# Kernel optimization log

Hardware: AMD Instinct MI355X
Metric: run time of the kernel (lower is better)

## Reference

```python
import jax, jax.numpy as jnp
import numpy as np

NQ = 8          # num_qubits
NL = 3          # num_layers
B = 65536       # batch size (vectorized over the original per-sample loop)
DIM = 2 ** NQ   # 256 state-vector amplitudes

# Pauli-Z eigenvalues per qubit over the computational basis (wire 0 = MSB,
# matching pennylane default.qubit ordering): ZV[q, idx] in {+1, -1}.
_idx = np.arange(DIM)
ZV = np.stack([1.0 - 2.0 * ((_idx >> (NQ - 1 - q)) & 1) for q in range(NQ)]).astype(np.float32)  # (NQ, DIM)
ZZ = ZV[:-1] * ZV[1:]   # (NQ-1, DIM): Z_i Z_{i+1} diagonal for the CNOT-RZ-CNOT (=RZZ) blocks


def setup_inputs() -> dict:
    key = jax.random.key(0)
    k1, k2, k3 = jax.random.split(key, 3)
    # weights ~ U(-pi, pi), matching torch.rand(...)*2*pi - pi
    weights = jax.random.uniform(k1, (NL, 2 * NQ - 1), minval=-np.pi, maxval=np.pi, dtype=jnp.float32)
    # latent noise ~ U(-1, 1), matching torch.rand(batch)*2 - 1
    z1 = jax.random.uniform(k2, (B,), minval=-1.0, maxval=1.0, dtype=jnp.float32)
    z2 = jax.random.uniform(k3, (B,), minval=-1.0, maxval=1.0, dtype=jnp.float32)
    return {"weights": weights, "z1": z1, "z2": z2}


def _apply_ry(state, theta, q):
    """Apply RY(theta) on wire q of state shaped (B, 2, ..., 2)."""
    half = theta * 0.5
    co, si = jnp.cos(half), jnp.sin(half)
    U = jnp.stack([jnp.stack([co, -si]), jnp.stack([si, co])]).astype(state.dtype)  # (2,2)
    s = jnp.moveaxis(state, q + 1, -1)
    s = s @ U.T
    return jnp.moveaxis(s, -1, q + 1)


def _circuit(weights, z1, z2):
    # Initial layer: per qubit RY(arcsin(z1)) then RZ(arcsin(z2)) on |0>
    # -> single-qubit state [e^{-i a2/2} cos(a1/2), e^{+i a2/2} sin(a1/2)], identical on all wires.
    a1 = jnp.arcsin(z1)
    a2 = jnp.arcsin(z2)
    ph = jnp.exp(-0.5j * a2)                              # (B,) complex64
    v = jnp.stack([ph * jnp.cos(0.5 * a1),
                   jnp.conj(ph) * jnp.sin(0.5 * a1)], axis=-1).astype(jnp.complex64)  # (B, 2)
    # Product state across NQ wires: (B, 2^NQ)
    state = v
    for _ in range(NQ - 1):
        state = (state[:, :, None] * v[:, None, :]).reshape(state.shape[0], -1)
    state = state.reshape((-1,) + (2,) * NQ)

    zz = jnp.asarray(ZZ)
    for l in range(NL):
        for q in range(NQ):
            state = _apply_ry(state, weights[l, q], q)
        # Entangling block: CNOT(i,i+1) RZ(w) CNOT(i,i+1) == RZZ(w) on (i,i+1),
        # all diagonal -> fuse the whole block into one phase multiply.
        angle = weights[l, NQ:] @ zz                      # (DIM,)
        diag = jnp.exp(-0.5j * angle).reshape((2,) * NQ)
        state = state * diag

    probs = jnp.abs(state.reshape(state.shape[0], -1)) ** 2   # (B, DIM)
    return (probs @ jnp.asarray(ZV).T).astype(jnp.float32)    # (B, NQ) <Z_q> expectations


def reference(weights, z1, z2):
    return _circuit(weights, z1, z2)
```

## Files before the change

kernel.cpp:

```cpp
#include <hip/hip_runtime.h>


#define ROW 92

template <int CTRL>
__device__ __forceinline__ float dppf(float x) {
    return __int_as_float(
        __builtin_amdgcn_mov_dpp(__float_as_int(x), CTRL, 0xF, 0xF, true));
}
template <int PAT>
__device__ __forceinline__ float swzp(float x) {
    return __int_as_float(__builtin_amdgcn_ds_swizzle(__float_as_int(x), PAT));
}
template <int B>
__device__ __forceinline__ float lane_xor(float x) {
    if constexpr (B == 0) return dppf<0xB1>(x);
    else if constexpr (B == 1) return dppf<0x4E>(x);
    else if constexpr (B == 2) return swzp<0x101F>(x);
    else if constexpr (B == 3) return dppf<0x128>(x);
    else if constexpr (B == 4) return swzp<0x401F>(x);
    else return __shfl_xor(x, 32, 64);
}

__device__ __forceinline__ void gate_lds2_5(float2 Cv[5], float2 (*xch)[256],
                                            float2 cs0, float2 cs1,
                                            int j, int M0) {
    __syncthreads();
    #pragma unroll
    for (int m = 0; m < 5; ++m) xch[M0 + m][j] = Cv[m];
    __syncthreads();
    const float s0 = (j & 128) ? cs0.y : -cs0.y;
    const float s1 = (j & 64)  ? cs1.y : -cs1.y;
    const float a00 = cs0.x * cs1.x, a01 = cs0.x * s1;
    const float a10 = s0 * cs1.x,    a11 = s0 * s1;
    #pragma unroll
    for (int m = 0; m < 5; ++m) {
        const float2 p01 = xch[M0 + m][j ^ 64];
        const float2 p10 = xch[M0 + m][j ^ 128];
        const float2 p11 = xch[M0 + m][j ^ 192];
        Cv[m].x = a00 * Cv[m].x + a01 * p01.x + a10 * p10.x + a11 * p11.x;
        Cv[m].y = a00 * Cv[m].y + a01 * p01.y + a10 * p10.y + a11 * p11.y;
    }
}

template <int B>
__device__ __forceinline__ void gate_wave5(float2 Cv[5], float2 cs, int j) {
    const float sg = ((j >> B) & 1) ? cs.y : -cs.y;
    #pragma unroll
    for (int m = 0; m < 5; ++m) {
        const float pr = lane_xor<B>(Cv[m].x);
        const float pi = lane_xor<B>(Cv[m].y);
        Cv[m].x = cs.x * Cv[m].x + sg * pr;
        Cv[m].y = cs.x * Cv[m].y + sg * pi;
    }
}

template <int N>
__device__ __forceinline__ void wht_chunk(float (&v)[N], float* buf,
                                          int lane, int wvg, int row, int base) {
    #define WHT_LVL(B)                                                   \
    {                                                                    \
        const float sgn = ((lane >> (B)) & 1) ? -1.f : 1.f;              \
        _Pragma("unroll")                                                \
        for (int i = 0; i < N; ++i) {                                    \
            const float p = lane_xor<B>(v[i]);                           \
            v[i] = fmaf(sgn, v[i], p);                                   \
        }                                                                \
    }
    WHT_LVL(0) WHT_LVL(1) WHT_LVL(2) WHT_LVL(3) WHT_LVL(4) WHT_LVL(5)
    #undef WHT_LVL
    if (row >= 0) {
        #pragma unroll
        for (int i = 0; i < N; ++i) buf[(wvg * 7 + row) * 81 + base + i] = v[i];
    }
}

template <int D, int N>
__device__ __forceinline__ void fill_pairs(const float2 (&C9)[9], float (&c)[N],
                                           int off) {
    #pragma unroll
    for (int k = 0; k + D <= 8; ++k) {
        const float2 hi = C9[k + D], lo = C9[k];
        c[off + 2 * k]     = 2.f * (hi.x * lo.x + hi.y * lo.y);
        c[off + 2 * k + 1] = 2.f * (hi.y * lo.x - hi.x * lo.y);
    }
}

__device__ __forceinline__ void prep(float z1v, float z2v, float& u, float& w8,
                                     float Tr[9], float Ti[9]) {
    const float u1 = sqrtf(fmaxf(0.f, 1.f - z1v * z1v));
    const float q1 = 0.5f * (1.f + u1);
    const float s1 = copysignf(sqrtf(fmaxf(0.f, 0.5f * (1.f - u1))), z1v);
    const float tn = s1 * rsqrtf(q1);
    const float u2 = sqrtf(fmaxf(0.f, 1.f - z2v * z2v));
    const float tr = tn * u2, ti = tn * z2v;
    u = tn * tn;
    w8 = q1 * q1; w8 *= w8; w8 *= w8;
    Tr[1] = tr; Ti[1] = ti;
    #pragma unroll
    for (int d = 2; d <= 8; ++d) {
        Tr[d] = Tr[d - 1] * tr - Ti[d - 1] * ti;
        Ti[d] = Tr[d - 1] * ti + Ti[d - 1] * tr;
    }
}

__device__ __forceinline__ float apoly1(const float* gp, float u) {
    const float4 c0 = ((const float4*)gp)[0];
    const float4 c1 = ((const float4*)gp)[1];
    const float4 c2 = ((const float4*)gp)[2];
    const float a[9] = {c0.x, c0.y, c0.z, c0.w, c1.x, c1.y, c1.z, c1.w, c2.x};
    float r = a[8];
    #pragma unroll
    for (int m = 7; m >= 0; --m) r = fmaf(r, u, a[m]);
    return r;
}

template <int NP>
__device__ __forceinline__ float2 bpoly1(const float* gp, float u) {
    constexpr int NF4 = (2 * NP + 3) / 4;
    float4 c[NF4];
    const float4* p = (const float4*)gp;
    #pragma unroll
    for (int i = 0; i < NF4; ++i) c[i] = p[i];
    float br = 0.f, bi = 0.f;
    #pragma unroll
    for (int k = NP - 1; k >= 0; --k) {
        const float re = (k & 1) ? c[k >> 1].z : c[k >> 1].x;
        const float im = (k & 1) ? c[k >> 1].w : c[k >> 1].y;
        br = fmaf(br, u, re);
        bi = fmaf(bi, u, im);
    }
    return make_float2(br, bi);
}

__global__ __launch_bounds__(512, 2)
void qsim_fused(const float* __restrict__ w, const float* __restrict__ z1,
                const float* __restrict__ z2, float* __restrict__ out,
                int nsamp) {
    __shared__ float2 xch[9][256];
    __shared__ float2 s_cs[3][8];
    __shared__ __align__(16) float g[8 * ROW];

    const int t = threadIdx.x;
    const int j = t & 255;
    const int h = t >> 8;
    const int M0 = h * 4;
    const int lane = t & 63, wvg = (t >> 6) & 3;

    const int s = blockIdx.x * 256 + j;
    const bool ev = (s < nsamp);
    float u = 0.f, w8 = 0.f;
    float Tr[9], Ti[9];
    if (ev) prep(z1[s], z2[s], u, w8, Tr, Ti);

    if (t < 24) {
        int l = t >> 3, q = t & 7;
        float a = 0.5f * w[l * 15 + q];
        s_cs[l][q] = make_float2(__cosf(a), __sinf(a));
    }
    __syncthreads();

    float2 Cv[5];
    #pragma unroll
    for (int m = 0; m < 5; ++m)
        Cv[m] = make_float2((__popc(j) == M0 + m) ? 1.f : 0.f, 0.f);

    for (int l = 0; l < 3; ++l) {
        gate_lds2_5(Cv, xch, s_cs[l][0], s_cs[l][1], j, M0);
        gate_wave5<5>(Cv, s_cs[l][2], j);
        gate_wave5<4>(Cv, s_cs[l][3], j);
        gate_wave5<3>(Cv, s_cs[l][4], j);
        gate_wave5<2>(Cv, s_cs[l][5], j);
        gate_wave5<1>(Cv, s_cs[l][6], j);
        gate_wave5<0>(Cv, s_cs[l][7], j);
        if (l < 2) {
            float ang = 0.f;
            #pragma unroll
            for (int i = 0; i < 7; ++i) {
                float zz = (((j >> (7 - i)) ^ (j >> (6 - i))) & 1) ? -1.f : 1.f;
                ang = fmaf(w[l * 15 + 8 + i], zz, ang);
            }
            float s2, c2;
            __sincosf(0.5f * ang, &s2, &c2);
            #pragma unroll
            for (int m = 0; m < 5; ++m) {
                const float nr = Cv[m].x * c2 + Cv[m].y * s2;
                const float ni = Cv[m].y * c2 - Cv[m].x * s2;
                Cv[m].x = nr; Cv[m].y = ni;
            }
        }
    }

    __syncthreads();
    #pragma unroll
    for (int m = 0; m < 5; ++m) xch[M0 + m][j] = Cv[m];
    __syncthreads();
    float2 C9[9];
    #pragma unroll
    for (int m = 0; m < 9; ++m) C9[m] = xch[m][j];
    __syncthreads();

    float* buf = (float*)xch + h * (28 * 81);
    const int row = (lane == 0) ? 0 : (lane == 1) ? 1 : (lane == 2) ? 2 :
                    (lane == 4) ? 3 : (lane == 8) ? 4 : (lane == 16) ? 5 :
                    (lane == 32) ? 6 : -1;
    if (h == 0) {
        {   float c[9];
            #pragma unroll
            for (int m = 0; m < 9; ++m)
                c[m] = C9[m].x * C9[m].x + C9[m].y * C9[m].y;
            wht_chunk(c, buf, lane, wvg, row, 0);
        }
        { float c[16]; fill_pairs<1>(C9, c, 0); wht_chunk(c, buf, lane, wvg, row, 9);  }
        { float c[14]; fill_pairs<2>(C9, c, 0); wht_chunk(c, buf, lane, wvg, row, 25); }
    } else {
        { float c[12]; fill_pairs<3>(C9, c, 0); wht_chunk(c, buf, lane, wvg, row, 39); }
        { float c[10]; fill_pairs<4>(C9, c, 0); wht_chunk(c, buf, lane, wvg, row, 51); }
        { float c[8];  fill_pairs<5>(C9, c, 0); wht_chunk(c, buf, lane, wvg, row, 61); }
        {   float c[12];
            fill_pairs<6>(C9, c, 0);
            fill_pairs<7>(C9, c, 6);
            fill_pairs<8>(C9, c, 10);
            wht_chunk(c, buf, lane, wvg, row, 69);
        }
    }
    __syncthreads();
    for (int o = t; o < 648; o += 512) {
        const int q = o / 81, i = o - 81 * q;
        const int b = 7 - q;
        const float* gb = (const float*)xch + ((i < 39) ? 0 : 28 * 81);
        float r;
        if (b < 6) {
            const int rw = b + 1;
            r = gb[(0 * 7 + rw) * 81 + i] + gb[(1 * 7 + rw) * 81 + i] +
                gb[(2 * 7 + rw) * 81 + i] + gb[(3 * 7 + rw) * 81 + i];
        } else if (b == 6) {
            r = gb[(0 * 7) * 81 + i] - gb[(1 * 7) * 81 + i] +
                gb[(2 * 7) * 81 + i] - gb[(3 * 7) * 81 + i];
        } else {
            r = gb[(0 * 7) * 81 + i] + gb[(1 * 7) * 81 + i] -
                gb[(2 * 7) * 81 + i] - gb[(3 * 7) * 81 + i];
        }
        const int off = i + ((i < 9) ? 0 : (i < 39) ? 3 : (i < 61) ? 5 :
                             (i < 75) ? 7 : 9);
        g[q * ROW + off] = r;
    }
    __syncthreads();

    if (!ev) return;

    float o4[4];
    #pragma unroll
    for (int qq = 0; qq < 4; ++qq) {
        const float* gq = g + (M0 + qq) * ROW;
        float r = apoly1(gq, u);
        #define DTERM(D, NP, OFF)                                        \
        {                                                                \
            const float2 b = bpoly1<NP>(gq + OFF, u);                    \
            r = fmaf(Tr[D], b.x, r);                                     \
            r = fmaf(-Ti[D], b.y, r);                                    \
        }
        DTERM(1, 8, 12) DTERM(2, 7, 28) DTERM(3, 6, 44) DTERM(4, 5, 56)
        DTERM(5, 4, 68) DTERM(6, 3, 76) DTERM(7, 2, 84) DTERM(8, 1, 88)
        #undef DTERM
        o4[qq] = w8 * r;
    }

    float4* op = (float4*)(out + (size_t)s * 8 + M0);
    *op = make_float4(o4[0], o4[1], o4[2], o4[3]);
}

extern "C" void kernel_launch(void* const* d_in, const int* in_sizes, int n_in,
                              void* d_out, int out_size, void* d_ws,
                              size_t ws_size, hipStream_t stream) {
    const float* w  = (const float*)d_in[0];
    const float* z1 = (const float*)d_in[1];
    const float* z2 = (const float*)d_in[2];
    float* out = (float*)d_out;

    const int n = in_sizes[1];
    qsim_fused<<<(n + 255) / 256, 512, 0, stream>>>(w, z1, z2, out, n);
}
```

Measured before the change: 16.30 us.

## Split work across four 256-thread groups with 1024-thread blocks

Raises the block size from 512 to 1024 threads so each group of 256 threads carries fewer Hamming-weight slices (3 instead of 5) during the gate simulation. The Walsh-Hadamard chunks are redistributed over four groups, and each thread evaluates two output qubits instead of four. The per-sample prep is moved after the reduction so fewer registers stay live. This adds per-thread parallelism and cuts register pressure, but it duplicates some work (the slice arrays overlap between groups), makes launch bounds much tighter, and uses larger blocks with more barrier participants.

```diff
diff --git a/kernel.cpp b/kernel.cpp
--- a/kernel.cpp
+++ b/kernel.cpp
@@ -22,19 +22,19 @@
     else return __shfl_xor(x, 32, 64);
 }
 
-__device__ __forceinline__ void gate_lds2_5(float2 Cv[5], float2 (*xch)[256],
+__device__ __forceinline__ void gate_lds2_3(float2 Cv[3], float2 (*xch)[256],
                                             float2 cs0, float2 cs1,
                                             int j, int M0) {
     __syncthreads();
     #pragma unroll
-    for (int m = 0; m < 5; ++m) xch[M0 + m][j] = Cv[m];
+    for (int m = 0; m < 3; ++m) xch[M0 + m][j] = Cv[m];
     __syncthreads();
     const float s0 = (j & 128) ? cs0.y : -cs0.y;
     const float s1 = (j & 64)  ? cs1.y : -cs1.y;
     const float a00 = cs0.x * cs1.x, a01 = cs0.x * s1;
     const float a10 = s0 * cs1.x,    a11 = s0 * s1;
     #pragma unroll
-    for (int m = 0; m < 5; ++m) {
+    for (int m = 0; m < 3; ++m) {
         const float2 p01 = xch[M0 + m][j ^ 64];
         const float2 p10 = xch[M0 + m][j ^ 128];
         const float2 p11 = xch[M0 + m][j ^ 192];
@@ -44,10 +44,10 @@
 }
 
 template <int B>
-__device__ __forceinline__ void gate_wave5(float2 Cv[5], float2 cs, int j) {
+__device__ __forceinline__ void gate_wave3(float2 Cv[3], float2 cs, int j) {
     const float sg = ((j >> B) & 1) ? cs.y : -cs.y;
     #pragma unroll
-    for (int m = 0; m < 5; ++m) {
+    for (int m = 0; m < 3; ++m) {
         const float pr = lane_xor<B>(Cv[m].x);
         const float pi = lane_xor<B>(Cv[m].y);
         Cv[m].x = cs.x * Cv[m].x + sg * pr;
@@ -133,7 +133,7 @@
     return make_float2(br, bi);
 }
 
-__global__ __launch_bounds__(512, 2)
+__global__ __launch_bounds__(1024, 4)
 void qsim_fused(const float* __restrict__ w, const float* __restrict__ z1,
                 const float* __restrict__ z2, float* __restrict__ out,
                 int nsamp) {
@@ -144,14 +144,13 @@
     const int t = threadIdx.x;
     const int j = t & 255;
     const int h = t >> 8;
-    const int M0 = h * 4;
+    const int M0 = 2 * h;
     const int lane = t & 63, wvg = (t >> 6) & 3;
 
     const int s = blockIdx.x * 256 + j;
     const bool ev = (s < nsamp);
-    float u = 0.f, w8 = 0.f;
-    float Tr[9], Ti[9];
-    if (ev) prep(z1[s], z2[s], u, w8, Tr, Ti);
+    const float z1v = ev ? z1[s] : 0.f;
+    const float z2v = ev ? z2[s] : 0.f;
 
     if (t < 24) {
         int l = t >> 3, q = t & 7;
@@ -160,19 +159,19 @@
     }
     __syncthreads();
 
-    float2 Cv[5];
-    #pragma unroll
-    for (int m = 0; m < 5; ++m)
+    float2 Cv[3];
+    #pragma unroll
+    for (int m = 0; m < 3; ++m)
         Cv[m] = make_float2((__popc(j) == M0 + m) ? 1.f : 0.f, 0.f);
 
     for (int l = 0; l < 3; ++l) {
-        gate_lds2_5(Cv, xch, s_cs[l][0], s_cs[l][1], j, M0);
-        gate_wave5<5>(Cv, s_cs[l][2], j);
-        gate_wave5<4>(Cv, s_cs[l][3], j);
-        gate_wave5<3>(Cv, s_cs[l][4], j);
-        gate_wave5<2>(Cv, s_cs[l][5], j);
-        gate_wave5<1>(Cv, s_cs[l][6], j);
-        gate_wave5<0>(Cv, s_cs[l][7], j);
+        gate_lds2_3(Cv, xch, s_cs[l][0], s_cs[l][1], j, M0);
+        gate_wave3<5>(Cv, s_cs[l][2], j);
+        gate_wave3<4>(Cv, s_cs[l][3], j);
+        gate_wave3<3>(Cv, s_cs[l][4], j);
+        gate_wave3<2>(Cv, s_cs[l][5], j);
+        gate_wave3<1>(Cv, s_cs[l][6], j);
+        gate_wave3<0>(Cv, s_cs[l][7], j);
         if (l < 2) {
             float ang = 0.f;
             #pragma unroll
@@ -183,7 +182,7 @@
             float s2, c2;
             __sincosf(0.5f * ang, &s2, &c2);
             #pragma unroll
-            for (int m = 0; m < 5; ++m) {
+            for (int m = 0; m < 3; ++m) {
                 const float nr = Cv[m].x * c2 + Cv[m].y * s2;
                 const float ni = Cv[m].y * c2 - Cv[m].x * s2;
                 Cv[m].x = nr; Cv[m].y = ni;
@@ -193,14 +192,14 @@
 
     __syncthreads();
     #pragma unroll
-    for (int m = 0; m < 5; ++m) xch[M0 + m][j] = Cv[m];
+    for (int m = 0; m < 3; ++m) xch[M0 + m][j] = Cv[m];
     __syncthreads();
     float2 C9[9];
     #pragma unroll
     for (int m = 0; m < 9; ++m) C9[m] = xch[m][j];
     __syncthreads();
 
-    float* buf = (float*)xch + h * (28 * 81);
+    float* buf = (float*)xch;
     const int row = (lane == 0) ? 0 : (lane == 1) ? 1 : (lane == 2) ? 2 :
                     (lane == 4) ? 3 : (lane == 8) ? 4 : (lane == 16) ? 5 :
                     (lane == 32) ? 6 : -1;
@@ -211,35 +210,34 @@
                 c[m] = C9[m].x * C9[m].x + C9[m].y * C9[m].y;
             wht_chunk(c, buf, lane, wvg, row, 0);
         }
+        { float c[12]; fill_pairs<3>(C9, c, 0); wht_chunk(c, buf, lane, wvg, row, 39); }
+    } else if (h == 1) {
         { float c[16]; fill_pairs<1>(C9, c, 0); wht_chunk(c, buf, lane, wvg, row, 9);  }
+        { float c[2];  fill_pairs<8>(C9, c, 0); wht_chunk(c, buf, lane, wvg, row, 79); }
+    } else if (h == 2) {
         { float c[14]; fill_pairs<2>(C9, c, 0); wht_chunk(c, buf, lane, wvg, row, 25); }
+        { float c[6];  fill_pairs<6>(C9, c, 0); wht_chunk(c, buf, lane, wvg, row, 69); }
     } else {
-        { float c[12]; fill_pairs<3>(C9, c, 0); wht_chunk(c, buf, lane, wvg, row, 39); }
         { float c[10]; fill_pairs<4>(C9, c, 0); wht_chunk(c, buf, lane, wvg, row, 51); }
         { float c[8];  fill_pairs<5>(C9, c, 0); wht_chunk(c, buf, lane, wvg, row, 61); }
-        {   float c[12];
-            fill_pairs<6>(C9, c, 0);
-            fill_pairs<7>(C9, c, 6);
-            fill_pairs<8>(C9, c, 10);
-            wht_chunk(c, buf, lane, wvg, row, 69);
-        }
-    }
-    __syncthreads();
-    for (int o = t; o < 648; o += 512) {
+        { float c[4];  fill_pairs<7>(C9, c, 0); wht_chunk(c, buf, lane, wvg, row, 75); }
+    }
+    __syncthreads();
+    if (t < 648) {
+        const int o = t;
         const int q = o / 81, i = o - 81 * q;
         const int b = 7 - q;
-        const float* gb = (const float*)xch + ((i < 39) ? 0 : 28 * 81);
         float r;
         if (b < 6) {
             const int rw = b + 1;
-            r = gb[(0 * 7 + rw) * 81 + i] + gb[(1 * 7 + rw) * 81 + i] +
-                gb[(2 * 7 + rw) * 81 + i] + gb[(3 * 7 + rw) * 81 + i];
+            r = buf[(0 * 7 + rw) * 81 + i] + buf[(1 * 7 + rw) * 81 + i] +
+                buf[(2 * 7 + rw) * 81 + i] + buf[(3 * 7 + rw) * 81 + i];
         } else if (b == 6) {
-            r = gb[(0 * 7) * 81 + i] - gb[(1 * 7) * 81 + i] +
-                gb[(2 * 7) * 81 + i] - gb[(3 * 7) * 81 + i];
+            r = buf[(0 * 7) * 81 + i] - buf[(1 * 7) * 81 + i] +
+                buf[(2 * 7) * 81 + i] - buf[(3 * 7) * 81 + i];
         } else {
-            r = gb[(0 * 7) * 81 + i] + gb[(1 * 7) * 81 + i] -
-                gb[(2 * 7) * 81 + i] - gb[(3 * 7) * 81 + i];
+            r = buf[(0 * 7) * 81 + i] + buf[(1 * 7) * 81 + i] -
+                buf[(2 * 7) * 81 + i] - buf[(3 * 7) * 81 + i];
         }
         const int off = i + ((i < 9) ? 0 : (i < 39) ? 3 : (i < 61) ? 5 :
                              (i < 75) ? 7 : 9);
@@ -249,10 +247,14 @@
 
     if (!ev) return;
 
-    float o4[4];
-    #pragma unroll
-    for (int qq = 0; qq < 4; ++qq) {
-        const float* gq = g + (M0 + qq) * ROW;
+    float u, w8;
+    float Tr[9], Ti[9];
+    prep(z1v, z2v, u, w8, Tr, Ti);
+
+    float o2[2];
+    #pragma unroll
+    for (int k = 0; k < 2; ++k) {
+        const float* gq = g + (M0 + k) * ROW;
         float r = apoly1(gq, u);
         #define DTERM(D, NP, OFF)                                        \
         {                                                                \
@@ -263,11 +265,11 @@
         DTERM(1, 8, 12) DTERM(2, 7, 28) DTERM(3, 6, 44) DTERM(4, 5, 56)
         DTERM(5, 4, 68) DTERM(6, 3, 76) DTERM(7, 2, 84) DTERM(8, 1, 88)
         #undef DTERM
-        o4[qq] = w8 * r;
-    }
-
-    float4* op = (float4*)(out + (size_t)s * 8 + M0);
-    *op = make_float4(o4[0], o4[1], o4[2], o4[3]);
+        o2[k] = w8 * r;
+    }
+
+    float2* op = (float2*)(out + (size_t)s * 8 + M0);
+    *op = make_float2(o2[0], o2[1]);
 }
 
 extern "C" void kernel_launch(void* const* d_in, const int* in_sizes, int n_in,
@@ -279,5 +281,5 @@
     float* out = (float*)d_out;
 
     const int n = in_sizes[1];
-    qsim_fused<<<(n + 255) / 256, 512, 0, stream>>>(w, z1, z2, out, n);
-}
+    qsim_fused<<<(n + 255) / 256, 1024, 0, stream>>>(w, z1, z2, out, n);
+}
```

Measured after the change: 16.77 us. 2.9% more time.

## Remap final polynomial stage to one qubit per thread over four samples

Applied to the files above, without the earlier changes.

The final evaluation stage is remapped so each thread handles one qubit for four consecutive samples, instead of four qubits for one sample. The thread loads that qubit's coefficient row from shared memory into registers once and reuses it for all four samples. z1/z2 are now read as float4 vectors and the per-sample prep is recomputed four times per thread. The cost is about four times more redundant prep work, a 92-float register array under a 512x2 launch bound (risk of spills), and narrower scattered output stores. A partially filled last group of four samples would see zero inputs rather than the real ones.

```diff
diff --git a/kernel.cpp b/kernel.cpp
--- a/kernel.cpp
+++ b/kernel.cpp
@@ -104,35 +104,6 @@
     }
 }
 
-__device__ __forceinline__ float apoly1(const float* gp, float u) {
-    const float4 c0 = ((const float4*)gp)[0];
-    const float4 c1 = ((const float4*)gp)[1];
-    const float4 c2 = ((const float4*)gp)[2];
-    const float a[9] = {c0.x, c0.y, c0.z, c0.w, c1.x, c1.y, c1.z, c1.w, c2.x};
-    float r = a[8];
-    #pragma unroll
-    for (int m = 7; m >= 0; --m) r = fmaf(r, u, a[m]);
-    return r;
-}
-
-template <int NP>
-__device__ __forceinline__ float2 bpoly1(const float* gp, float u) {
-    constexpr int NF4 = (2 * NP + 3) / 4;
-    float4 c[NF4];
-    const float4* p = (const float4*)gp;
-    #pragma unroll
-    for (int i = 0; i < NF4; ++i) c[i] = p[i];
-    float br = 0.f, bi = 0.f;
-    #pragma unroll
-    for (int k = NP - 1; k >= 0; --k) {
-        const float re = (k & 1) ? c[k >> 1].z : c[k >> 1].x;
-        const float im = (k & 1) ? c[k >> 1].w : c[k >> 1].y;
-        br = fmaf(br, u, re);
-        bi = fmaf(bi, u, im);
-    }
-    return make_float2(br, bi);
-}
-
 __global__ __launch_bounds__(512, 2)
 void qsim_fused(const float* __restrict__ w, const float* __restrict__ z1,
                 const float* __restrict__ z2, float* __restrict__ out,
@@ -147,11 +118,15 @@
     const int M0 = h * 4;
     const int lane = t & 63, wvg = (t >> 6) & 3;
 
-    const int s = blockIdx.x * 256 + j;
-    const bool ev = (s < nsamp);
-    float u = 0.f, w8 = 0.f;
-    float Tr[9], Ti[9];
-    if (ev) prep(z1[s], z2[s], u, w8, Tr, Ti);
+    const int gidx = t >> 3;
+    const int sbase = blockIdx.x * 256 + gidx * 4;
+    const bool ev4 = (sbase + 3 < nsamp);
+    float4 z1v4 = make_float4(0.f, 0.f, 0.f, 0.f);
+    float4 z2v4 = z1v4;
+    if (ev4) {
+        z1v4 = *(const float4*)(z1 + sbase);
+        z2v4 = *(const float4*)(z2 + sbase);
+    }
 
     if (t < 24) {
         int l = t >> 3, q = t & 7;
@@ -247,27 +222,58 @@
     }
     __syncthreads();
 
-    if (!ev) return;
-
+    const int q = t & 7;
+    const float* gq = g + q * ROW;
+
+    float a[ROW];
+    #pragma unroll
+    for (int i = 0; i < 23; ++i) {
+        const float4 c = ((const float4*)gq)[i];
+        a[4 * i + 0] = c.x; a[4 * i + 1] = c.y;
+        a[4 * i + 2] = c.z; a[4 * i + 3] = c.w;
+    }
+
+    const float z1a[4] = {z1v4.x, z1v4.y, z1v4.z, z1v4.w};
+    const float z2a[4] = {z2v4.x, z2v4.y, z2v4.z, z2v4.w};
     float o4[4];
-    #pragma unroll
-    for (int qq = 0; qq < 4; ++qq) {
-        const float* gq = g + (M0 + qq) * ROW;
-        float r = apoly1(gq, u);
+
+    #pragma unroll
+    for (int i = 0; i < 4; ++i) {
+        float u, w8;
+        float Tr[9], Ti[9];
+        prep(z1a[i], z2a[i], u, w8, Tr, Ti);
+
+        float r = a[8];
+        #pragma unroll
+        for (int m = 7; m >= 0; --m) r = fmaf(r, u, a[m]);
+
         #define DTERM(D, NP, OFF)                                        \
         {                                                                \
-            const float2 b = bpoly1<NP>(gq + OFF, u);                    \
-            r = fmaf(Tr[D], b.x, r);                                     \
-            r = fmaf(-Ti[D], b.y, r);                                    \
+            float br = a[OFF + 2 * (NP - 1)];                            \
+            float bi = a[OFF + 2 * (NP - 1) + 1];                        \
+            _Pragma("unroll")                                            \
+            for (int k = NP - 2; k >= 0; --k) {                          \
+                br = fmaf(br, u, a[OFF + 2 * k]);                        \
+                bi = fmaf(bi, u, a[OFF + 2 * k + 1]);                    \
+            }                                                            \
+            r = fmaf(Tr[D], br, r);                                      \
+            r = fmaf(-Ti[D], bi, r);                                     \
         }
         DTERM(1, 8, 12) DTERM(2, 7, 28) DTERM(3, 6, 44) DTERM(4, 5, 56)
         DTERM(5, 4, 68) DTERM(6, 3, 76) DTERM(7, 2, 84) DTERM(8, 1, 88)
         #undef DTERM
-        o4[qq] = w8 * r;
-    }
-
-    float4* op = (float4*)(out + (size_t)s * 8 + M0);
-    *op = make_float4(o4[0], o4[1], o4[2], o4[3]);
+        o4[i] = w8 * r;
+    }
+
+    if (ev4) {
+        #pragma unroll
+        for (int i = 0; i < 4; ++i)
+            out[(size_t)(sbase + i) * 8 + q] = o4[i];
+    } else {
+        #pragma unroll
+        for (int i = 0; i < 4; ++i)
+            if (sbase + i < nsamp) out[(size_t)(sbase + i) * 8 + q] = o4[i];
+    }
 }
 
 extern "C" void kernel_launch(void* const* d_in, const int* in_sizes, int n_in,
```

Measured after the change: 16.27 us. Within noise of the previous version (-0.2%).

## Distribute weight-polynomial state evolution over nine waves with in-register qubit pairs

Applied to the files above, without the earlier changes.

Restructures the circuit-evolution stage so each of nine waves (576 threads) owns one Hamming-weight column and holds four amplitudes per lane. The top two qubits are applied in registers via pair rotations instead of an LDS exchange with two barriers per layer. The ZZ phase is built from precomputed cos/sin products rather than an angle sum plus sincos. Per-sample prep is also deferred until after the shared reduction, which lowers register pressure during evolution. This removes per-layer syncthreads and redundant five-slot work per thread, at the cost of a larger block, a separate WHT buffer in LDS, and an idle 9th wave in later phases.

```diff
diff --git a/kernel.cpp b/kernel.cpp
--- a/kernel.cpp
+++ b/kernel.cpp
@@ -22,37 +22,27 @@
     else return __shfl_xor(x, 32, 64);
 }
 
-__device__ __forceinline__ void gate_lds2_5(float2 Cv[5], float2 (*xch)[256],
-                                            float2 cs0, float2 cs1,
-                                            int j, int M0) {
-    __syncthreads();
-    #pragma unroll
-    for (int m = 0; m < 5; ++m) xch[M0 + m][j] = Cv[m];
-    __syncthreads();
-    const float s0 = (j & 128) ? cs0.y : -cs0.y;
-    const float s1 = (j & 64)  ? cs1.y : -cs1.y;
-    const float a00 = cs0.x * cs1.x, a01 = cs0.x * s1;
-    const float a10 = s0 * cs1.x,    a11 = s0 * s1;
-    #pragma unroll
-    for (int m = 0; m < 5; ++m) {
-        const float2 p01 = xch[M0 + m][j ^ 64];
-        const float2 p10 = xch[M0 + m][j ^ 128];
-        const float2 p11 = xch[M0 + m][j ^ 192];
-        Cv[m].x = a00 * Cv[m].x + a01 * p01.x + a10 * p10.x + a11 * p11.x;
-        Cv[m].y = a00 * Cv[m].y + a01 * p01.y + a10 * p10.y + a11 * p11.y;
-    }
+__device__ __forceinline__ float2 cmul(float2 a, float2 b) {
+    return make_float2(a.x * b.x - a.y * b.y, a.x * b.y + a.y * b.x);
 }
 
 template <int B>
-__device__ __forceinline__ void gate_wave5(float2 Cv[5], float2 cs, int j) {
-    const float sg = ((j >> B) & 1) ? cs.y : -cs.y;
-    #pragma unroll
-    for (int m = 0; m < 5; ++m) {
-        const float pr = lane_xor<B>(Cv[m].x);
-        const float pi = lane_xor<B>(Cv[m].y);
-        Cv[m].x = cs.x * Cv[m].x + sg * pr;
-        Cv[m].y = cs.x * Cv[m].y + sg * pi;
-    }
+__device__ __forceinline__ void gate_lane(float2 CA[4], float2 cs, int lane) {
+    const float sg = ((lane >> B) & 1) ? cs.y : -cs.y;
+    #pragma unroll
+    for (int r = 0; r < 4; ++r) {
+        const float px = lane_xor<B>(CA[r].x);
+        const float py = lane_xor<B>(CA[r].y);
+        CA[r].x = cs.x * CA[r].x + sg * px;
+        CA[r].y = cs.x * CA[r].y + sg * py;
+    }
+}
+__device__ __forceinline__ void gate_pair(float2& a0, float2& a1, float2 cs) {
+    const float2 t0 = make_float2(cs.x * a0.x - cs.y * a1.x,
+                                  cs.x * a0.y - cs.y * a1.y);
+    const float2 t1 = make_float2(cs.y * a0.x + cs.x * a1.x,
+                                  cs.y * a0.y + cs.x * a1.y);
+    a0 = t0; a1 = t1;
 }
 
 template <int N>
@@ -133,102 +123,114 @@
     return make_float2(br, bi);
 }
 
-__global__ __launch_bounds__(512, 2)
+__global__ __launch_bounds__(576, 3)
 void qsim_fused(const float* __restrict__ w, const float* __restrict__ z1,
                 const float* __restrict__ z2, float* __restrict__ out,
                 int nsamp) {
-    __shared__ float2 xch[9][256];
-    __shared__ float2 s_cs[3][8];
+    __shared__ float2 xchC[9][256];
+    __shared__ float wht[2 * 28 * 81];
+    __shared__ float2 s_cs[3][15];
     __shared__ __align__(16) float g[8 * ROW];
 
     const int t = threadIdx.x;
+    const int lane = t & 63;
+    const int wv = t >> 6;
     const int j = t & 255;
-    const int h = t >> 8;
+    const int h = (t >> 8) & 1;
     const int M0 = h * 4;
-    const int lane = t & 63, wvg = (t >> 6) & 3;
 
     const int s = blockIdx.x * 256 + j;
-    const bool ev = (s < nsamp);
-    float u = 0.f, w8 = 0.f;
-    float Tr[9], Ti[9];
-    if (ev) prep(z1[s], z2[s], u, w8, Tr, Ti);
-
-    if (t < 24) {
-        int l = t >> 3, q = t & 7;
-        float a = 0.5f * w[l * 15 + q];
-        s_cs[l][q] = make_float2(__cosf(a), __sinf(a));
-    }
-    __syncthreads();
-
-    float2 Cv[5];
-    #pragma unroll
-    for (int m = 0; m < 5; ++m)
-        Cv[m] = make_float2((__popc(j) == M0 + m) ? 1.f : 0.f, 0.f);
-
+    const bool ev = (t < 512) && (s < nsamp);
+    const float z1v = ev ? z1[s] : 0.f;
+    const float z2v = ev ? z2[s] : 0.f;
+
+    if (t < 45) {
+        const int l = t / 15, i = t - 15 * l;
+        const float a = 0.5f * w[l * 15 + i];
+        s_cs[l][i] = make_float2(__cosf(a), __sinf(a));
+    }
+    __syncthreads();
+
+    float2 CA[4];
+    const int pl = __popc(lane);
+    #pragma unroll
+    for (int r = 0; r < 4; ++r)
+        CA[r] = make_float2((pl + (r >> 1) + (r & 1) == wv) ? 1.f : 0.f, 0.f);
+
+    #pragma unroll 1
     for (int l = 0; l < 3; ++l) {
-        gate_lds2_5(Cv, xch, s_cs[l][0], s_cs[l][1], j, M0);
-        gate_wave5<5>(Cv, s_cs[l][2], j);
-        gate_wave5<4>(Cv, s_cs[l][3], j);
-        gate_wave5<3>(Cv, s_cs[l][4], j);
-        gate_wave5<2>(Cv, s_cs[l][5], j);
-        gate_wave5<1>(Cv, s_cs[l][6], j);
-        gate_wave5<0>(Cv, s_cs[l][7], j);
+        gate_pair(CA[0], CA[2], s_cs[l][0]);
+        gate_pair(CA[1], CA[3], s_cs[l][0]);
+        gate_pair(CA[0], CA[1], s_cs[l][1]);
+        gate_pair(CA[2], CA[3], s_cs[l][1]);
+        gate_lane<5>(CA, s_cs[l][2], lane);
+        gate_lane<4>(CA, s_cs[l][3], lane);
+        gate_lane<3>(CA, s_cs[l][4], lane);
+        gate_lane<2>(CA, s_cs[l][5], lane);
+        gate_lane<1>(CA, s_cs[l][6], lane);
+        gate_lane<0>(CA, s_cs[l][7], lane);
         if (l < 2) {
-            float ang = 0.f;
+            float2 base = make_float2(1.f, 0.f);
             #pragma unroll
-            for (int i = 0; i < 7; ++i) {
-                float zz = (((j >> (7 - i)) ^ (j >> (6 - i))) & 1) ? -1.f : 1.f;
-                ang = fmaf(w[l * 15 + 8 + i], zz, ang);
-            }
-            float s2, c2;
-            __sincosf(0.5f * ang, &s2, &c2);
+            for (int i = 2; i <= 6; ++i) {
+                const float2 cz = s_cs[l][8 + i];
+                const int d = ((lane >> (7 - i)) ^ (lane >> (6 - i))) & 1;
+                base = cmul(base, make_float2(cz.x, d ? cz.y : -cz.y));
+            }
+            const float2 cz0 = s_cs[l][8];
+            const float2 cz1 = s_cs[l][9];
+            const int l5 = (lane >> 5) & 1;
             #pragma unroll
-            for (int m = 0; m < 5; ++m) {
-                const float nr = Cv[m].x * c2 + Cv[m].y * s2;
-                const float ni = Cv[m].y * c2 - Cv[m].x * s2;
-                Cv[m].x = nr; Cv[m].y = ni;
-            }
-        }
-    }
-
-    __syncthreads();
-    #pragma unroll
-    for (int m = 0; m < 5; ++m) xch[M0 + m][j] = Cv[m];
-    __syncthreads();
-    float2 C9[9];
-    #pragma unroll
-    for (int m = 0; m < 9; ++m) C9[m] = xch[m][j];
-    __syncthreads();
-
-    float* buf = (float*)xch + h * (28 * 81);
-    const int row = (lane == 0) ? 0 : (lane == 1) ? 1 : (lane == 2) ? 2 :
-                    (lane == 4) ? 3 : (lane == 8) ? 4 : (lane == 16) ? 5 :
-                    (lane == 32) ? 6 : -1;
-    if (h == 0) {
-        {   float c[9];
-            #pragma unroll
-            for (int m = 0; m < 9; ++m)
-                c[m] = C9[m].x * C9[m].x + C9[m].y * C9[m].y;
-            wht_chunk(c, buf, lane, wvg, row, 0);
-        }
-        { float c[16]; fill_pairs<1>(C9, c, 0); wht_chunk(c, buf, lane, wvg, row, 9);  }
-        { float c[14]; fill_pairs<2>(C9, c, 0); wht_chunk(c, buf, lane, wvg, row, 25); }
-    } else {
-        { float c[12]; fill_pairs<3>(C9, c, 0); wht_chunk(c, buf, lane, wvg, row, 39); }
-        { float c[10]; fill_pairs<4>(C9, c, 0); wht_chunk(c, buf, lane, wvg, row, 51); }
-        { float c[8];  fill_pairs<5>(C9, c, 0); wht_chunk(c, buf, lane, wvg, row, 61); }
-        {   float c[12];
-            fill_pairs<6>(C9, c, 0);
-            fill_pairs<7>(C9, c, 6);
-            fill_pairs<8>(C9, c, 10);
-            wht_chunk(c, buf, lane, wvg, row, 69);
-        }
-    }
-    __syncthreads();
-    for (int o = t; o < 648; o += 512) {
+            for (int r = 0; r < 4; ++r) {
+                const int d0 = ((r >> 1) ^ (r & 1)) & 1;
+                const int d1 = (r & 1) ^ l5;
+                float2 ph = cmul(base, make_float2(cz0.x, d0 ? cz0.y : -cz0.y));
+                ph = cmul(ph, make_float2(cz1.x, d1 ? cz1.y : -cz1.y));
+                CA[r] = cmul(CA[r], ph);
+            }
+        }
+    }
+
+    #pragma unroll
+    for (int r = 0; r < 4; ++r) xchC[wv][r * 64 + lane] = CA[r];
+    __syncthreads();
+
+    const int wvg = (t >> 6) & 3;
+    if (t < 512) {
+        float2 C9[9];
+        #pragma unroll
+        for (int m = 0; m < 9; ++m) C9[m] = xchC[m][j];
+        float* buf = wht + h * (28 * 81);
+        const int row = (lane == 0) ? 0 : (lane == 1) ? 1 : (lane == 2) ? 2 :
+                        (lane == 4) ? 3 : (lane == 8) ? 4 : (lane == 16) ? 5 :
+                        (lane == 32) ? 6 : -1;
+        if (h == 0) {
+            {   float c[9];
+                #pragma unroll
+                for (int m = 0; m < 9; ++m)
+                    c[m] = C9[m].x * C9[m].x + C9[m].y * C9[m].y;
+                wht_chunk(c, buf, lane, wvg, row, 0);
+            }
+            { float c[16]; fill_pairs<1>(C9, c, 0); wht_chunk(c, buf, lane, wvg, row, 9);  }
+            { float c[14]; fill_pairs<2>(C9, c, 0); wht_chunk(c, buf, lane, wvg, row, 25); }
+        } else {
+            { float c[12]; fill_pairs<3>(C9, c, 0); wht_chunk(c, buf, lane, wvg, row, 39); }
+            { float c[10]; fill_pairs<4>(C9, c, 0); wht_chunk(c, buf, lane, wvg, row, 51); }
+            { float c[8];  fill_pairs<5>(C9, c, 0); wht_chunk(c, buf, lane, wvg, row, 61); }
+            {   float c[12];
+                fill_pairs<6>(C9, c, 0);
+                fill_pairs<7>(C9, c, 6);
+                fill_pairs<8>(C9, c, 10);
+                wht_chunk(c, buf, lane, wvg, row, 69);
+            }
+        }
+    }
+    __syncthreads();
+
+    for (int o = t; o < 648; o += 576) {
         const int q = o / 81, i = o - 81 * q;
         const int b = 7 - q;
-        const float* gb = (const float*)xch + ((i < 39) ? 0 : 28 * 81);
+        const float* gb = wht + ((i < 39) ? 0 : 28 * 81);
         float r;
         if (b < 6) {
             const int rw = b + 1;
@@ -249,10 +251,14 @@
 
     if (!ev) return;
 
+    float u, w8;
+    float Tr[9], Ti[9];
+    prep(z1v, z2v, u, w8, Tr, Ti);
+
     float o4[4];
     #pragma unroll
-    for (int qq = 0; qq < 4; ++qq) {
-        const float* gq = g + (M0 + qq) * ROW;
+    for (int k = 0; k < 4; ++k) {
+        const float* gq = g + (M0 + k) * ROW;
         float r = apoly1(gq, u);
         #define DTERM(D, NP, OFF)                                        \
         {                                                                \
@@ -263,7 +269,7 @@
         DTERM(1, 8, 12) DTERM(2, 7, 28) DTERM(3, 6, 44) DTERM(4, 5, 56)
         DTERM(5, 4, 68) DTERM(6, 3, 76) DTERM(7, 2, 84) DTERM(8, 1, 88)
         #undef DTERM
-        o4[qq] = w8 * r;
+        o4[k] = w8 * r;
     }
 
     float4* op = (float4*)(out + (size_t)s * 8 + M0);
@@ -279,5 +285,5 @@
     float* out = (float*)d_out;
 
     const int n = in_sizes[1];
-    qsim_fused<<<(n + 255) / 256, 512, 0, stream>>>(w, z1, z2, out, n);
-}
+    qsim_fused<<<(n + 255) / 256, 576, 0, stream>>>(w, z1, z2, out, n);
+}
```

Result: no change. 16.29 us (-0.0%).
